# Kernel tuning notes

Measured on AMD Instinct MI355X. Metric: run time of the kernel, lower is better.

Reference implementation:

```python
import jax, jax.numpy as jnp
import numpy as np

N, D_IN, D_OUT, E = 8192, 2048, 2048, 8


def setup_inputs() -> dict:
    key = jax.random.key(0)
    k0, k1, k2, k3, k4, k5 = jax.random.split(key, 6)
    s = 1.0 / np.sqrt(D_IN)  # torch nn.Linear default init range
    return {
        "inputs": jax.random.normal(k0, (N, D_IN), jnp.float32),
        "condition": jax.random.normal(k1, (N, D_IN), jnp.float32),
        "Wp": jax.random.uniform(k2, (E, D_IN), jnp.float32, -s, s),
        "bp": jax.random.uniform(k3, (E,), jnp.float32, -s, s),
        "We": jax.random.uniform(k4, (E, D_OUT, D_IN), jnp.float32, -s, s),
        "be": jax.random.uniform(k5, (E, D_OUT), jnp.float32, -s, s),
    }


def reference(inputs, condition, Wp, bp, We, be):
    # predictor: gating logits [N, E]
    prediction = condition @ Wp.T + bp
    # straight-through multiplier: value == 1, gradient flows to prediction
    multiply = jnp.ones_like(prediction) + (prediction - jax.lax.stop_gradient(prediction))
    # run ALL experts on the full batch (faithful to the original): [E, N, F]
    expert_out = jnp.einsum('nd,efd->enf', inputs, We) + be[:, None, :]
    combined = multiply.T[:, :, None] * expert_out  # [E, N, F]
    # select the argmax expert per row
    idx = jnp.argmax(prediction, axis=-1)  # [N]
    result = combined[idx, jnp.arange(prediction.shape[0])]  # [N, F]
    return result
```

## Files before the change

### kernel.cpp

```cpp
#include <hip/hip_runtime.h>
#include <hip/hip_bf16.h>
#include <stdint.h>

#define N_ROWS 8192
#define DIN 2048
#define DOUT 2048
#define NE 8

#define BM3 320
#define BN3 256
#define BK2 64
#define RT3 33
#define NBLK3 (8 * RT3)

#define BM 128
#define BN 128
#define BK 64
#define MAX_RT 71

typedef __bf16 bf16x8 __attribute__((ext_vector_type(8)));
typedef float f32x4 __attribute__((ext_vector_type(4)));

__device__ __forceinline__ uint32_t f2bf(float f) {
  uint32_t u = __builtin_bit_cast(uint32_t, f);
  uint32_t r = u + 0x7FFFu + ((u >> 16) & 1u);
  return r >> 16;
}

__device__ __forceinline__ void gl2lds16(const void* g, void* l) {
  __builtin_amdgcn_global_load_lds(
      (const __attribute__((address_space(1))) unsigned int*)g,
      (__attribute__((address_space(3))) unsigned int*)l, 16, 0, 0);
}

__global__ __launch_bounds__(256) void gate_kernel(
    const float* __restrict__ cond, const float* __restrict__ Wp,
    const float* __restrict__ bp, const float* __restrict__ X,
    int* __restrict__ idx, int* __restrict__ counts, __hip_bfloat16* __restrict__ Xb)
{
  __shared__ int lc[NE];
  const int t = threadIdx.x;
  if (t < NE) lc[t] = 0;

  const int lane = t & 63;
  const int wid  = t >> 6;
  const int row  = blockIdx.x * 4 + wid;

  double acc[NE];
  #pragma unroll
  for (int e = 0; e < NE; ++e) acc[e] = 0.0;

  const float4* crow = (const float4*)(cond + (size_t)row * DIN);
  const float4* wp4  = (const float4*)Wp;
  #pragma unroll
  for (int i = 0; i < DIN / 256; ++i) {
    float4 c = crow[i * 64 + lane];
    #pragma unroll
    for (int e = 0; e < NE; ++e) {
      float4 w = wp4[e * (DIN / 4) + i * 64 + lane];
      acc[e] += (double)c.x * w.x + (double)c.y * w.y
              + (double)c.z * w.z + (double)c.w * w.w;
    }
  }
  #pragma unroll
  for (int e = 0; e < NE; ++e) {
    double v = acc[e];
    #pragma unroll
    for (int off = 32; off > 0; off >>= 1) v += __shfl_down(v, off, 64);
    acc[e] = v;
  }
  __syncthreads();
  if (lane == 0) {
    int best = 0; double bv = acc[0] + (double)bp[0];
    #pragma unroll
    for (int e = 1; e < NE; ++e) {
      double v = acc[e] + (double)bp[e];
      if (v > bv) { bv = v; best = e; }
    }
    idx[row] = best;
    atomicAdd(&lc[best], 1);
  }

  {
    const float4* xs = (const float4*)(X + (size_t)blockIdx.x * 4 * DIN);
    uint4* xd = (uint4*)(Xb + (size_t)blockIdx.x * 4 * DIN);
    #pragma unroll
    for (int c = 0; c < 4; ++c) {
      int ch = t + c * 256;
      float4 v0 = xs[ch * 2];
      float4 v1 = xs[ch * 2 + 1];
      uint4 o;
      o.x = f2bf(v0.x) | (f2bf(v0.y) << 16);
      o.y = f2bf(v0.z) | (f2bf(v0.w) << 16);
      o.z = f2bf(v1.x) | (f2bf(v1.y) << 16);
      o.w = f2bf(v1.z) | (f2bf(v1.w) << 16);
      xd[ch] = o;
    }
  }

  __syncthreads();
  if (t < NE && lc[t] > 0) atomicAdd(&counts[t], lc[t]);
}

__global__ void scan_kernel(const int* __restrict__ counts, int* __restrict__ offsets) {
  if (threadIdx.x == 0 && blockIdx.x == 0) {
    int s = 0;
    for (int e = 0; e < NE; ++e) { offsets[e] = s; s += counts[e]; }
  }
}

__global__ __launch_bounds__(256) void scatter_kernel(
    const int* __restrict__ idx, const int* __restrict__ offsets,
    int* __restrict__ fill, int* __restrict__ rows)
{
  __shared__ int lc[NE], lb[NE];
  const int t = threadIdx.x;
  if (t < NE) lc[t] = 0;
  __syncthreads();
  int n = blockIdx.x * 256 + t;
  int e = idx[n];
  int my = atomicAdd(&lc[e], 1);
  __syncthreads();
  if (t < NE) lb[t] = (lc[t] > 0) ? atomicAdd(&fill[t], lc[t]) : 0;
  __syncthreads();
  rows[offsets[e] + lb[e] + my] = n;
}

__global__ __launch_bounds__(256) void conv_kernel(
    const float* __restrict__ src, __hip_bfloat16* __restrict__ dst, size_t nchunks)
{
  const size_t stride = (size_t)gridDim.x * 256;
  for (size_t c = (size_t)blockIdx.x * 256 + threadIdx.x; c < nchunks; c += stride) {
    float4 v0 = ((const float4*)src)[c * 2];
    float4 v1 = ((const float4*)src)[c * 2 + 1];
    uint4 o;
    o.x = f2bf(v0.x) | (f2bf(v0.y) << 16);
    o.y = f2bf(v0.z) | (f2bf(v0.w) << 16);
    o.z = f2bf(v1.x) | (f2bf(v1.y) << 16);
    o.w = f2bf(v1.z) | (f2bf(v1.w) << 16);
    ((uint4*)dst)[c] = o;
  }
}

__global__ __launch_bounds__(512, 1) void moe_gemm8(
    const __hip_bfloat16* __restrict__ Xb, const __hip_bfloat16* __restrict__ Web,
    const float* __restrict__ be, const int* __restrict__ counts,
    const int* __restrict__ rows, float* __restrict__ out)
{
  __shared__ __align__(16) __hip_bfloat16 Asm[2][2][160 * 64];
  __shared__ __align__(16) __hip_bfloat16 Bsm[2][2][128 * 64];
  __shared__ int rowid[BM3];

  const int bid = blockIdx.x;
  const int w = (bid & 7) * RT3 + (bid >> 3);
  const int ct = w / RT3;
  const int rt = w % RT3;

  int e = 0, racc = 0, cnt = 0, base = 0;
  for (; e < NE; ++e) {
    cnt = counts[e];
    int tiles = (cnt + BM3 - 1) / BM3;
    if (rt < racc + tiles) break;
    racc += tiles; base += cnt;
  }
  if (e == NE) return;
  const int row0 = (rt - racc) * BM3;
  const int tid = threadIdx.x;
  if (tid < BM3)
    rowid[tid] = (row0 + tid < cnt) ? rows[base + row0 + tid] : -1;
  __syncthreads();

  const int lane = tid & 63, wid = tid >> 6;
  const bool w4 = (wid < 4);
  const int wm = wid >> 2, wn = wid & 3;
  const int g = lane >> 4, fr = lane & 15;

  const int cA0 = w4 ? (3 * wid) : (12 + 2 * (wid - 4));
  const int cA1 = cA0 + 1;
  const int cA2 = cA0 + 2;
  const int cB0 = 2 * wid, cB1 = cB0 + 1;

  const int aD0 = cA0 * 1024 + lane * 16;
  const int aD1 = cA1 * 1024 + lane * 16;
  const int aD2 = cA2 * 1024 + lane * 16;
  const int bD0 = cB0 * 1024 + lane * 16;
  const int bD1 = cB1 * 1024 + lane * 16;

  const int frs = lane >> 2, q = lane & 3;
  const __hip_bfloat16 *aP[2][3], *bP[2][2];
  {
    const int cA[3] = {cA0, cA1, cA2};
    const int cB[2] = {cB0, cB1};
    #pragma unroll
    for (int h = 0; h < 2; ++h) {
      #pragma unroll
      for (int s = 0; s < 3; ++s) {
        int c = cA[s];
        int R = h * 160 + (c >> 1) * 16 + frs;
        int gr = rowid[R];
        if (gr < 0) gr = 0;
        aP[h][s] = Xb + (size_t)gr * DIN + (c & 1) * 32 + q * 8;
      }
      #pragma unroll
      for (int s = 0; s < 2; ++s) {
        int c = cB[s];
        size_t wrow = (size_t)e * DOUT + ct * BN3 + h * 128 + (c >> 1) * 16 + frs;
        bP[h][s] = Web + wrow * DIN + (c & 1) * 32 + q * 8;
      }
    }
  }

  f32x4 acc[2][2][5][2];
  #pragma unroll
  for (int a = 0; a < 2; ++a)
    #pragma unroll
    for (int b = 0; b < 2; ++b)
      #pragma unroll
      for (int m = 0; m < 5; ++m)
        #pragma unroll
        for (int n = 0; n < 2; ++n)
          acc[a][b][m][n] = 0.0f;

  bf16x8 av[2][5], bv[2][2];

#define STG_A(buf, h, kel) do {                                              \
    gl2lds16(aP[h][0] + (kel), (char*)&Asm[buf][h][0] + aD0);                \
    gl2lds16(aP[h][1] + (kel), (char*)&Asm[buf][h][0] + aD1);                \
    if (w4) gl2lds16(aP[h][2] + (kel), (char*)&Asm[buf][h][0] + aD2);        \
  } while (0)
#define STG_B(buf, h, kel) do {                                              \
    gl2lds16(bP[h][0] + (kel), (char*)&Bsm[buf][h][0] + bD0);                \
    gl2lds16(bP[h][1] + (kel), (char*)&Bsm[buf][h][0] + bD1); } while (0)

#define READ_A(c, h) do { const char* Ab_ = (const char*)&Asm[c][h][0];      \
    _Pragma("unroll") for (int kk = 0; kk < 2; ++kk)                         \
    _Pragma("unroll") for (int mi = 0; mi < 5; ++mi) {                       \
      int by = (wm * 5 + mi) * 2048 + kk * 1024 + fr * 64 + g * 16;          \
      av[kk][mi] = *(const bf16x8*)(Ab_ + by); } } while (0)

#define READ_B(c, h) do { const char* Bb_ = (const char*)&Bsm[c][h][0];      \
    _Pragma("unroll") for (int kk = 0; kk < 2; ++kk)                         \
    _Pragma("unroll") for (int ni = 0; ni < 2; ++ni) {                       \
      int by = (wn * 2 + ni) * 2048 + kk * 1024 + fr * 64 + g * 16;          \
      bv[kk][ni] = *(const bf16x8*)(Bb_ + by); } } while (0)

#define BAR   __builtin_amdgcn_s_barrier()
#define LGKM0 do { asm volatile("s_waitcnt lgkmcnt(0)" ::: "memory");        \
                   __builtin_amdgcn_sched_barrier(0); } while (0)
#define VMCN  do { if (w4) { asm volatile("s_waitcnt vmcnt(5)" ::: "memory"); } \
                   else    { asm volatile("s_waitcnt vmcnt(4)" ::: "memory"); } \
                   __builtin_amdgcn_sched_barrier(0); } while (0)
#define VMC0  do { asm volatile("s_waitcnt vmcnt(0)" ::: "memory");          \
                   __builtin_amdgcn_sched_barrier(0); } while (0)

#define MFMA_PH(mh, nh) do { __builtin_amdgcn_s_setprio(1);                  \
    _Pragma("unroll") for (int kk = 0; kk < 2; ++kk)                         \
    _Pragma("unroll") for (int mi = 0; mi < 5; ++mi)                         \
    _Pragma("unroll") for (int ni = 0; ni < 2; ++ni)                         \
      acc[mh][nh][mi][ni] = __builtin_amdgcn_mfma_f32_16x16x32_bf16(         \
          av[kk][mi], bv[kk][ni], acc[mh][nh][mi][ni], 0, 0, 0);             \
    __builtin_amdgcn_s_setprio(0); } while (0)

  STG_A(0, 0, 0);  STG_B(0, 0, 0);  STG_A(0, 1, 0);  STG_B(0, 1, 0);
  STG_A(1, 0, 64); STG_B(1, 0, 64);
  VMCN;
  BAR;

  const int T = DIN / BK2;
  #pragma unroll 1
  for (int t = 0; t < T; ++t) {
    const int c = t & 1, o = c ^ 1;
    const int k1 = (t + 1) * BK2, k2 = (t + 2) * BK2;
    const bool s1 = (t + 1 < T), s2 = (t + 2 < T);

    READ_A(c, 0); READ_B(c, 0);
    if (s1) STG_A(o, 1, k1);
    BAR; LGKM0;
    MFMA_PH(0, 0);
    BAR;

    READ_B(c, 1);
    if (s1) STG_B(o, 1, k1);
    BAR; LGKM0;
    MFMA_PH(0, 1);
    BAR;

    READ_A(c, 1); READ_B(c, 0);
    if (s2) STG_A(c, 0, k2);
    BAR; LGKM0;
    MFMA_PH(1, 0);
    BAR;

    READ_B(c, 1);
    if (s2) STG_B(c, 0, k2);
    BAR; LGKM0;
    MFMA_PH(1, 1);
    if (s2) { VMCN; } else { VMC0; }
    BAR;
  }

#undef STG_A
#undef STG_B
#undef READ_A
#undef READ_B
#undef MFMA_PH

  float beh[2][2];
  #pragma unroll
  for (int nh = 0; nh < 2; ++nh)
    #pragma unroll
    for (int ni = 0; ni < 2; ++ni)
      beh[nh][ni] = be[(size_t)e * DOUT + ct * BN3 + nh * 128 + wn * 32 + ni * 16 + fr];

  #pragma unroll
  for (int mh = 0; mh < 2; ++mh)
    #pragma unroll
    for (int mi = 0; mi < 5; ++mi)
      #pragma unroll
      for (int j = 0; j < 4; ++j) {
        int R = mh * 160 + wm * 80 + mi * 16 + g * 4 + j;
        int grow = rowid[R];
        if (grow < 0) continue;
        float* orow = out + (size_t)grow * DOUT + ct * BN3;
        #pragma unroll
        for (int nh = 0; nh < 2; ++nh)
          #pragma unroll
          for (int ni = 0; ni < 2; ++ni)
            orow[nh * 128 + wn * 32 + ni * 16 + fr] = acc[mh][nh][mi][ni][j] + beh[nh][ni];
      }
}

__global__ __launch_bounds__(256) void moe_gemm_fb(
    const float* __restrict__ X, const float* __restrict__ We,
    const float* __restrict__ be, const int* __restrict__ counts,
    const int* __restrict__ offsets, const int* __restrict__ rows,
    float* __restrict__ out)
{
  __shared__ __align__(16) unsigned char Asb[BM * BK * 2];
  __shared__ __align__(16) unsigned char Bsb[BN * BK * 2];
  __shared__ int rowid[BM];

  const int ct = blockIdx.x;
  const int rt = blockIdx.y;

  int e = 0, racc = 0, cnt = 0;
  for (; e < NE; ++e) {
    cnt = counts[e];
    int tiles = (cnt + BM - 1) / BM;
    if (rt < racc + tiles) break;
    racc += tiles;
  }
  if (e == NE) return;
  const int row0 = (rt - racc) * BM;
  const int base = offsets[e];

  if (threadIdx.x < BM) {
    int r = row0 + threadIdx.x;
    rowid[threadIdx.x] = (r < cnt) ? rows[base + r] : -1;
  }
  __syncthreads();

  const int t    = threadIdx.x;
  const int lane = t & 63;
  const int wv   = t >> 6;
  const int wr   = wv >> 1, wc = wv & 1;
  const int g    = lane >> 4, fr = lane & 15;
  const int srow = t >> 4;
  const int skq  = t & 15;

  f32x4 acc[4][4];
  #pragma unroll
  for (int m = 0; m < 4; ++m)
    #pragma unroll
    for (int n = 0; n < 4; ++n)
      acc[m][n] = 0.0f;

  const size_t bcol0 = (size_t)e * DOUT + (size_t)ct * BN;

  for (int k0 = 0; k0 < DIN; k0 += BK) {
    #pragma unroll
    for (int p = 0; p < 8; ++p) {
      int r = p * 16 + srow;
      int gr = rowid[r];
      float4 v = make_float4(0.f, 0.f, 0.f, 0.f);
      if (gr >= 0)
        v = *(const float4*)(X + (size_t)gr * DIN + k0 + skq * 4);
      uint32_t w0 = f2bf(v.x) | (f2bf(v.y) << 16);
      uint32_t w1 = f2bf(v.z) | (f2bf(v.w) << 16);
      int byte = r * (BK * 2) + ((skq * 8) ^ ((r & 7) << 4));
      *(uint2*)(Asb + byte) = make_uint2(w0, w1);
    }
    #pragma unroll
    for (int p = 0; p < 8; ++p) {
      int r = p * 16 + srow;
      float4 v = *(const float4*)(We + (bcol0 + r) * DIN + k0 + skq * 4);
      uint32_t w0 = f2bf(v.x) | (f2bf(v.y) << 16);
      uint32_t w1 = f2bf(v.z) | (f2bf(v.w) << 16);
      int byte = r * (BK * 2) + ((skq * 8) ^ ((r & 7) << 4));
      *(uint2*)(Bsb + byte) = make_uint2(w0, w1);
    }
    __syncthreads();

    #pragma unroll
    for (int kk = 0; kk < BK; kk += 32) {
      bf16x8 av[4], bv[4];
      #pragma unroll
      for (int m = 0; m < 4; ++m) {
        int r = wr * 64 + m * 16 + fr;
        int byte = r * (BK * 2) + ((((kk + g * 8) * 2)) ^ ((r & 7) << 4));
        av[m] = *(const bf16x8*)(Asb + byte);
      }
      #pragma unroll
      for (int n = 0; n < 4; ++n) {
        int c = wc * 64 + n * 16 + fr;
        int byte = c * (BK * 2) + ((((kk + g * 8) * 2)) ^ ((c & 7) << 4));
        bv[n] = *(const bf16x8*)(Bsb + byte);
      }
      #pragma unroll
      for (int m = 0; m < 4; ++m)
        #pragma unroll
        for (int n = 0; n < 4; ++n)
          acc[m][n] = __builtin_amdgcn_mfma_f32_16x16x32_bf16(av[m], bv[n], acc[m][n], 0, 0, 0);
    }
    __syncthreads();
  }

  const float* berow = be + (size_t)e * DOUT + (size_t)ct * BN + wc * 64;
  #pragma unroll
  for (int m = 0; m < 4; ++m) {
    #pragma unroll
    for (int j = 0; j < 4; ++j) {
      int r = wr * 64 + m * 16 + g * 4 + j;
      int grow = rowid[r];
      if (grow < 0) continue;
      float* orow = out + (size_t)grow * DOUT + (size_t)ct * BN + wc * 64;
      #pragma unroll
      for (int n = 0; n < 4; ++n)
        orow[n * 16 + fr] = acc[m][n][j] + berow[n * 16 + fr];
    }
  }
}

extern "C" void kernel_launch(void* const* d_in, const int* in_sizes, int n_in,
                              void* d_out, int out_size, void* d_ws, size_t ws_size,
                              hipStream_t stream) {
  const float* X    = (const float*)d_in[0];
  const float* cond = (const float*)d_in[1];
  const float* Wp   = (const float*)d_in[2];
  const float* bp   = (const float*)d_in[3];
  const float* We   = (const float*)d_in[4];
  const float* be   = (const float*)d_in[5];
  float* out = (float*)d_out;

  int* counts  = (int*)d_ws;
  int* offsets = counts + 8;
  int* fill    = counts + 16;
  int* idx     = (int*)((char*)d_ws + 256);
  int* rows    = idx + N_ROWS;
  const size_t XB_OFF  = 65792;
  const size_t WEB_OFF = XB_OFF + (size_t)N_ROWS * DIN * 2;
  const size_t WS_NEED = WEB_OFF + (size_t)NE * DOUT * DIN * 2;

  hipMemsetAsync(d_ws, 0, 256, stream);

  if (ws_size >= WS_NEED) {
    __hip_bfloat16* Xb  = (__hip_bfloat16*)((char*)d_ws + XB_OFF);
    __hip_bfloat16* Web = (__hip_bfloat16*)((char*)d_ws + WEB_OFF);
    gate_kernel<<<N_ROWS / 4, 256, 0, stream>>>(cond, Wp, bp, X, idx, counts, Xb);
    scan_kernel<<<1, 64, 0, stream>>>(counts, offsets);
    scatter_kernel<<<N_ROWS / 256, 256, 0, stream>>>(idx, offsets, fill, rows);
    conv_kernel<<<2048, 256, 0, stream>>>(We, Web, (size_t)NE * DOUT * DIN / 8);
    moe_gemm8<<<NBLK3, 512, 0, stream>>>(Xb, Web, be, counts, rows, out);
  } else {
    __hip_bfloat16* XbDummy = (__hip_bfloat16*)((char*)d_ws + 256 + 2 * N_ROWS * 4);
    gate_kernel<<<N_ROWS / 4, 256, 0, stream>>>(cond, Wp, bp, X, idx, counts, XbDummy);
    scan_kernel<<<1, 64, 0, stream>>>(counts, offsets);
    scatter_kernel<<<N_ROWS / 256, 256, 0, stream>>>(idx, offsets, fill, rows);
    moe_gemm_fb<<<dim3(DOUT / BN, MAX_RT), 256, 0, stream>>>(X, We, be, counts, offsets, rows, out);
  }
}
```

Baseline: 201.8 us.

## Fuse weight conversion into gate kernel and XOR-swizzle GEMM LDS tiles

The fp32-to-bf16 expert-weight conversion moves into the gate kernel as extra blocks, removing a separate launch and letting the conversion run alongside the gating work. Separately, the GEMM's global-to-LDS loads and LDS fragment reads use an XOR swizzle on the 16-byte column chunk to reduce LDS bank conflicts. The fused kernel gets a larger grid whose conversion blocks compete with gating blocks for bandwidth. The fallback path now passes null pointers so it skips both the Xb and weight conversion.

```diff
diff --git a/kernel.cpp b/kernel.cpp
--- a/kernel.cpp
+++ b/kernel.cpp
@@ -13,6 +13,9 @@
 #define RT3 33
 #define NBLK3 (8 * RT3)
 
+#define GATE_BLKS (N_ROWS / 4)
+#define CONV_BLKS 2560
+
 #define BM 128
 #define BN 128
 #define BK 64
@@ -33,13 +36,33 @@
       (__attribute__((address_space(3))) unsigned int*)l, 16, 0, 0);
 }
 
-__global__ __launch_bounds__(256) void gate_kernel(
+__global__ __launch_bounds__(256) void gate_conv_kernel(
     const float* __restrict__ cond, const float* __restrict__ Wp,
     const float* __restrict__ bp, const float* __restrict__ X,
-    int* __restrict__ idx, int* __restrict__ counts, __hip_bfloat16* __restrict__ Xb)
+    const float* __restrict__ We,
+    int* __restrict__ idx, int* __restrict__ counts,
+    __hip_bfloat16* __restrict__ Xb, __hip_bfloat16* __restrict__ Web)
 {
+  const int t = threadIdx.x;
+
+  if (blockIdx.x >= GATE_BLKS) {
+    if (!Web) return;
+    const size_t total = (size_t)NE * DOUT * DIN / 8;
+    const size_t stride = (size_t)CONV_BLKS * 256;
+    for (size_t c = (size_t)(blockIdx.x - GATE_BLKS) * 256 + t; c < total; c += stride) {
+      float4 v0 = ((const float4*)We)[c * 2];
+      float4 v1 = ((const float4*)We)[c * 2 + 1];
+      uint4 o;
+      o.x = f2bf(v0.x) | (f2bf(v0.y) << 16);
+      o.y = f2bf(v0.z) | (f2bf(v0.w) << 16);
+      o.z = f2bf(v1.x) | (f2bf(v1.y) << 16);
+      o.w = f2bf(v1.z) | (f2bf(v1.w) << 16);
+      ((uint4*)Web)[c] = o;
+    }
+    return;
+  }
+
   __shared__ int lc[NE];
-  const int t = threadIdx.x;
   if (t < NE) lc[t] = 0;
 
   const int lane = t & 63;
@@ -81,7 +104,7 @@
     atomicAdd(&lc[best], 1);
   }
 
-  {
+  if (Xb) {
     const float4* xs = (const float4*)(X + (size_t)blockIdx.x * 4 * DIN);
     uint4* xd = (uint4*)(Xb + (size_t)blockIdx.x * 4 * DIN);
     #pragma unroll
@@ -126,22 +149,6 @@
   rows[offsets[e] + lb[e] + my] = n;
 }
 
-__global__ __launch_bounds__(256) void conv_kernel(
-    const float* __restrict__ src, __hip_bfloat16* __restrict__ dst, size_t nchunks)
-{
-  const size_t stride = (size_t)gridDim.x * 256;
-  for (size_t c = (size_t)blockIdx.x * 256 + threadIdx.x; c < nchunks; c += stride) {
-    float4 v0 = ((const float4*)src)[c * 2];
-    float4 v1 = ((const float4*)src)[c * 2 + 1];
-    uint4 o;
-    o.x = f2bf(v0.x) | (f2bf(v0.y) << 16);
-    o.y = f2bf(v0.z) | (f2bf(v0.w) << 16);
-    o.z = f2bf(v1.x) | (f2bf(v1.y) << 16);
-    o.w = f2bf(v1.z) | (f2bf(v1.w) << 16);
-    ((uint4*)dst)[c] = o;
-  }
-}
-
 __global__ __launch_bounds__(512, 1) void moe_gemm8(
     const __hip_bfloat16* __restrict__ Xb, const __hip_bfloat16* __restrict__ Web,
     const float* __restrict__ be, const int* __restrict__ counts,
@@ -174,6 +181,7 @@
   const bool w4 = (wid < 4);
   const int wm = wid >> 2, wn = wid & 3;
   const int g = lane >> 4, fr = lane & 15;
+  const int rsw = fr * 64 + ((g ^ ((fr >> 1) & 3)) << 4);
 
   const int cA0 = w4 ? (3 * wid) : (12 + 2 * (wid - 4));
   const int cA1 = cA0 + 1;
@@ -186,7 +194,8 @@
   const int bD0 = cB0 * 1024 + lane * 16;
   const int bD1 = cB1 * 1024 + lane * 16;
 
-  const int frs = lane >> 2, q = lane & 3;
+  const int frs = lane >> 2;
+  const int qx  = (lane & 3) ^ ((lane >> 3) & 3);
   const __hip_bfloat16 *aP[2][3], *bP[2][2];
   {
     const int cA[3] = {cA0, cA1, cA2};
@@ -199,13 +208,13 @@
         int R = h * 160 + (c >> 1) * 16 + frs;
         int gr = rowid[R];
         if (gr < 0) gr = 0;
-        aP[h][s] = Xb + (size_t)gr * DIN + (c & 1) * 32 + q * 8;
+        aP[h][s] = Xb + (size_t)gr * DIN + (c & 1) * 32 + qx * 8;
       }
       #pragma unroll
       for (int s = 0; s < 2; ++s) {
         int c = cB[s];
         size_t wrow = (size_t)e * DOUT + ct * BN3 + h * 128 + (c >> 1) * 16 + frs;
-        bP[h][s] = Web + wrow * DIN + (c & 1) * 32 + q * 8;
+        bP[h][s] = Web + wrow * DIN + (c & 1) * 32 + qx * 8;
       }
     }
   }
@@ -234,15 +243,13 @@
 
 #define READ_A(c, h) do { const char* Ab_ = (const char*)&Asm[c][h][0];      \
     _Pragma("unroll") for (int kk = 0; kk < 2; ++kk)                         \
-    _Pragma("unroll") for (int mi = 0; mi < 5; ++mi) {                       \
-      int by = (wm * 5 + mi) * 2048 + kk * 1024 + fr * 64 + g * 16;          \
-      av[kk][mi] = *(const bf16x8*)(Ab_ + by); } } while (0)
+    _Pragma("unroll") for (int mi = 0; mi < 5; ++mi)                         \
+      av[kk][mi] = *(const bf16x8*)(Ab_ + (wm * 5 + mi) * 2048 + kk * 1024 + rsw); } while (0)
 
 #define READ_B(c, h) do { const char* Bb_ = (const char*)&Bsm[c][h][0];      \
     _Pragma("unroll") for (int kk = 0; kk < 2; ++kk)                         \
-    _Pragma("unroll") for (int ni = 0; ni < 2; ++ni) {                       \
-      int by = (wn * 2 + ni) * 2048 + kk * 1024 + fr * 64 + g * 16;          \
-      bv[kk][ni] = *(const bf16x8*)(Bb_ + by); } } while (0)
+    _Pragma("unroll") for (int ni = 0; ni < 2; ++ni)                         \
+      bv[kk][ni] = *(const bf16x8*)(Bb_ + (wn * 2 + ni) * 2048 + kk * 1024 + rsw); } while (0)
 
 #define BAR   __builtin_amdgcn_s_barrier()
 #define LGKM0 do { asm volatile("s_waitcnt lgkmcnt(0)" ::: "memory");        \
@@ -466,14 +473,14 @@
   if (ws_size >= WS_NEED) {
     __hip_bfloat16* Xb  = (__hip_bfloat16*)((char*)d_ws + XB_OFF);
     __hip_bfloat16* Web = (__hip_bfloat16*)((char*)d_ws + WEB_OFF);
-    gate_kernel<<<N_ROWS / 4, 256, 0, stream>>>(cond, Wp, bp, X, idx, counts, Xb);
+    gate_conv_kernel<<<GATE_BLKS + CONV_BLKS, 256, 0, stream>>>(
+        cond, Wp, bp, X, We, idx, counts, Xb, Web);
     scan_kernel<<<1, 64, 0, stream>>>(counts, offsets);
     scatter_kernel<<<N_ROWS / 256, 256, 0, stream>>>(idx, offsets, fill, rows);
-    conv_kernel<<<2048, 256, 0, stream>>>(We, Web, (size_t)NE * DOUT * DIN / 8);
     moe_gemm8<<<NBLK3, 512, 0, stream>>>(Xb, Web, be, counts, rows, out);
   } else {
-    __hip_bfloat16* XbDummy = (__hip_bfloat16*)((char*)d_ws + 256 + 2 * N_ROWS * 4);
-    gate_kernel<<<N_ROWS / 4, 256, 0, stream>>>(cond, Wp, bp, X, idx, counts, XbDummy);
+    gate_conv_kernel<<<GATE_BLKS + CONV_BLKS, 256, 0, stream>>>(
+        cond, Wp, bp, X, We, idx, counts, nullptr, nullptr);
     scan_kernel<<<1, 64, 0, stream>>>(counts, offsets);
     scatter_kernel<<<N_ROWS / 256, 256, 0, stream>>>(idx, offsets, fill, rows);
     moe_gemm_fb<<<dim3(DOUT / BN, MAX_RT), 256, 0, stream>>>(X, We, be, counts, offsets, rows, out);
```

Measured after the change: 190.9 us. 1.06x faster.
